# Kernel optimization log

Measured on AMD Instinct MI355X. Metric: run time of the kernel, lower is better.

The kernel has to match this reference:

```python
import jax, jax.numpy as jnp
import numpy as np

N_EMBD, D_INNER, DT_RANK, D_CONV, D_STATE, SEQ_LEN = 2048, 4096, 128, 4, 16, 2048


def setup_inputs() -> dict:
    key = jax.random.key(0)
    ks = jax.random.split(key, 8)
    sc = lambda fan_in: 1.0 / np.sqrt(fan_in)
    x = jax.random.normal(ks[0], (SEQ_LEN, N_EMBD), dtype=jnp.float32)
    in_proj_w = jax.random.normal(ks[1], (2 * D_INNER, N_EMBD), jnp.float32) * sc(N_EMBD)
    in_proj_b = jnp.zeros((2 * D_INNER,), jnp.float32)
    conv_w = jax.random.normal(ks[2], (D_INNER, 1, D_CONV), jnp.float32) * sc(D_CONV)
    conv_b = jnp.zeros((D_INNER,), jnp.float32)
    ssm_in_w = jax.random.normal(ks[3], (DT_RANK + 2 * D_STATE, D_INNER), jnp.float32) * sc(D_INNER)
    delta_w = jax.random.normal(ks[4], (D_INNER, DT_RANK), jnp.float32) * sc(DT_RANK)
    # A_log init exactly as module: repeat(arange(1,d_state+1), d_inner).reshape(d_inner,d_state)
    A_log = jnp.log(jnp.repeat(jnp.arange(1, D_STATE + 1), D_INNER).reshape(D_INNER, D_STATE).astype(jnp.float32))
    D = jnp.ones((D_INNER,), jnp.float32)
    out_w = jax.random.normal(ks[5], (N_EMBD, D_INNER), jnp.float32) * sc(D_INNER)
    out_b = jnp.zeros((N_EMBD,), jnp.float32)
    return {"x": x, "in_proj_w": in_proj_w, "in_proj_b": in_proj_b, "conv_w": conv_w,
            "conv_b": conv_b, "ssm_in_w": ssm_in_w, "delta_w": delta_w, "A_log": A_log,
            "D": D, "out_w": out_w, "out_b": out_b}


def selective_scan(u, delta, A, B, C, D):
    # u, delta: (L, di); A: (di, ds); B, C: (L, ds); D: (di,)
    dA = jnp.exp(delta[:, :, None] * A[None, :, :])                # (L, di, ds)
    dBu = delta[:, :, None] * B[:, None, :] * u[:, :, None]        # (L, di, ds)

    def step(h, inp):
        dA_t, dBu_t, C_t = inp
        h = dA_t * h + dBu_t                                       # (di, ds)
        y = jnp.einsum('ds,s->d', h, C_t)
        return h, y

    h0 = jnp.zeros((u.shape[1], A.shape[1]), u.dtype)
    _, ys = jax.lax.scan(step, h0, (dA, dBu, C))
    return ys + u * D                                              # (L, di)


def mamba_block(x, in_proj_w, in_proj_b, conv_w, conv_b, ssm_in_w, delta_w, A_log, D, out_w, out_b):
    L = x.shape[0]
    xr = x @ in_proj_w.T + in_proj_b                               # (L, 2*di)
    xi, res = jnp.split(xr, 2, axis=-1)
    # depthwise causal conv1d: left-pad d_conv-1 (== first L outputs of symmetric pad)
    xc = jax.lax.conv_general_dilated(
        xi.T[None],                                                # (1, di, L)
        conv_w,                                                    # (di, 1, k)
        window_strides=(1,), padding=[(D_CONV - 1, 0)],
        feature_group_count=D_INNER)[0] + conv_b[:, None]
    xc = jax.nn.silu(xc.T)                                         # (L, di)
    # SSM
    A = -jnp.exp(A_log)
    dbc = xc @ ssm_in_w.T                                          # (L, dt_rank + 2*ds)
    delta, B, C = jnp.split(dbc, [DT_RANK, DT_RANK + D_STATE], axis=-1)
    delta = jax.nn.softplus(delta @ delta_w.T)                     # (L, di)
    y = selective_scan(xc, delta, A, B, C, D)
    y = y * jax.nn.silu(res)
    return y @ out_w.T + out_b                                     # (L, n_embd)


def reference(x, in_proj_w, in_proj_b, conv_w, conv_b, ssm_in_w, delta_w, A_log, D, out_w, out_b):
    return mamba_block(x, in_proj_w, in_proj_b, conv_w, conv_b, ssm_in_w, delta_w, A_log, D, out_w, out_b)
```

## Files before the change

### kernel.cpp

```cpp
#include <hip/hip_runtime.h>
#include <cstdint>
#include <cstddef>


typedef __bf16 bf16x8 __attribute__((ext_vector_type(8)));
typedef float f32x4 __attribute__((ext_vector_type(4)));

#define GLDS16(g, l)                                        \
  __builtin_amdgcn_global_load_lds(                         \
      (__attribute__((address_space(1))) void*)(g),         \
      (__attribute__((address_space(3))) void*)(l), 16, 0, 0)

#define FENCE() asm volatile("" ::: "memory")
#define BARRIER()                      \
  do {                                 \
    FENCE();                           \
    __builtin_amdgcn_s_barrier();      \
    FENCE();                           \
  } while (0)

static __device__ __forceinline__ unsigned short f2b(float f) {
  unsigned int x = __builtin_bit_cast(unsigned int, f);
  x += 0x7fffu + ((x >> 16) & 1u);
  return (unsigned short)(x >> 16);
}

static __device__ __forceinline__ float b2f(unsigned short u) {
  return __builtin_bit_cast(float, (unsigned int)u << 16);
}

static __device__ __forceinline__ float sigmoidf_fast(float x) {
  return 1.0f / (1.0f + __expf(-x));
}

struct CastArgs {
  const float* src[5];
  unsigned short* dst[5];
  int n4[5];
};

__global__ __launch_bounds__(256) void cast_multi(CastArgs a) {
  const int stride = gridDim.x * 256;
  const int t = blockIdx.x * 256 + threadIdx.x;
#pragma unroll
  for (int k = 0; k < 5; ++k) {
    const float4* src = reinterpret_cast<const float4*>(a.src[k]);
    ushort4* dst = reinterpret_cast<ushort4*>(a.dst[k]);
    const int n4 = a.n4[k];
    for (int i = t; i < n4; i += stride) {
      float4 v = src[i];
      ushort4 o;
      o.x = f2b(v.x); o.y = f2b(v.y); o.z = f2b(v.z); o.w = f2b(v.w);
      dst[i] = o;
    }
  }
}

template <int MODE>
__global__ __launch_bounds__(512) void gemm256_bt(
    const unsigned short* __restrict__ A, const unsigned short* __restrict__ B,
    float* __restrict__ Cp, unsigned short* __restrict__ xib,
    unsigned short* __restrict__ rsb, const float* __restrict__ bias,
    int M, int N, int K, int Kslice) {
  __shared__ __align__(16) unsigned short lds[65536];
  const int tid = threadIdx.x;
  const int l = tid & 63;
  const int w = tid >> 6;
  const int wr = w >> 2;
  const int wc = w & 3;

  const int nwg = gridDim.x * gridDim.y;
  const int q = nwg >> 3;
  int flat = blockIdx.x + gridDim.x * blockIdx.y;
  flat = (flat & 7) * q + (flat >> 3);
  const int bx = flat % gridDim.x;
  const int by = flat / gridDim.x;

  const long brow = (long)bx * 256;
  const long bcol = (long)by * 256;
  const int ks = blockIdx.z;
  const int NT = Kslice >> 6;

  f32x4 acc[8][4] = {};

  const unsigned short* Ab = A + (size_t)brow * K + (size_t)ks * Kslice;
  const unsigned short* Bb = B + (size_t)bcol * K + (size_t)ks * Kslice;
  size_t soff[4];
  int doff[4];
#pragma unroll
  for (int i = 0; i < 4; ++i) {
    int idx = i * 512 + tid;
    int r = idx >> 3, s = idx & 7;
    soff[i] = (size_t)r * K + (size_t)((s ^ (r & 7)) << 3);
    doff[i] = idx * 8;
  }

  auto stage = [&](int kt, int buf) {
    const int k0 = kt << 6;
#pragma unroll
    for (int i = 0; i < 4; ++i)
      GLDS16(Ab + soff[i] + k0, &lds[buf * 32768 + doff[i]]);
#pragma unroll
    for (int i = 0; i < 4; ++i)
      GLDS16(Bb + soff[i] + k0, &lds[buf * 32768 + 16384 + doff[i]]);
  };

  const int hi = l >> 4, lo7 = l & 7;
  const int sw0 = ((0 + hi) ^ lo7) << 3;
  const int sw1 = ((4 + hi) ^ lo7) << 3;
  const int rowA = wr * 128 + (l & 15);
  const int colB = wc * 64 + (l & 15);

  stage(0, 0);
  stage(1, 1);

  int buf = 0;
  for (int kt = 0; kt < NT; ++kt) {
    const bool last = (kt == NT - 1);
    if (last) {
      asm volatile("s_waitcnt vmcnt(0)" ::: "memory");
    } else {
      asm volatile("s_waitcnt vmcnt(8)" ::: "memory");
    }
    BARRIER();
    const int bb = buf * 32768;
    bf16x8 a0[8], b0[4];
#pragma unroll
    for (int m = 0; m < 8; ++m)
      a0[m] = *reinterpret_cast<const bf16x8*>(&lds[bb + (rowA + m * 16) * 64 + sw0]);
#pragma unroll
    for (int n = 0; n < 4; ++n)
      b0[n] = *reinterpret_cast<const bf16x8*>(&lds[bb + 16384 + (colB + n * 16) * 64 + sw0]);
    __builtin_amdgcn_s_setprio(1);
#pragma unroll
    for (int m = 0; m < 8; ++m)
#pragma unroll
      for (int n = 0; n < 4; ++n)
        acc[m][n] = __builtin_amdgcn_mfma_f32_16x16x32_bf16(a0[m], b0[n], acc[m][n], 0, 0, 0);
    __builtin_amdgcn_s_setprio(0);
    bf16x8 a1[8], b1[4];
#pragma unroll
    for (int m = 0; m < 8; ++m)
      a1[m] = *reinterpret_cast<const bf16x8*>(&lds[bb + (rowA + m * 16) * 64 + sw1]);
#pragma unroll
    for (int n = 0; n < 4; ++n)
      b1[n] = *reinterpret_cast<const bf16x8*>(&lds[bb + 16384 + (colB + n * 16) * 64 + sw1]);
    asm volatile("s_waitcnt lgkmcnt(0)" ::: "memory");
    __builtin_amdgcn_sched_barrier(0);
    BARRIER();
    if (kt + 2 < NT) stage(kt + 2, buf);
    __builtin_amdgcn_s_setprio(1);
#pragma unroll
    for (int m = 0; m < 8; ++m)
#pragma unroll
      for (int n = 0; n < 4; ++n)
        acc[m][n] = __builtin_amdgcn_mfma_f32_16x16x32_bf16(a1[m], b1[n], acc[m][n], 0, 0, 0);
    __builtin_amdgcn_s_setprio(0);
    buf ^= 1;
  }

  const long r0 = brow + wr * 128 + (l >> 4) * 4;
  const long c0 = bcol + wc * 64 + (l & 15);
  if (MODE == 1) {
    float* Cb = Cp + (size_t)ks * M * N;
#pragma unroll
    for (int m = 0; m < 8; ++m)
#pragma unroll
      for (int n = 0; n < 4; ++n) {
        long col = c0 + n * 16;
#pragma unroll
        for (int r = 0; r < 4; ++r)
          Cb[(r0 + m * 16 + r) * (long)N + col] = acc[m][n][r];
      }
  } else {
#pragma unroll
    for (int m = 0; m < 8; ++m)
#pragma unroll
      for (int n = 0; n < 4; ++n) {
        long col = c0 + n * 16;
        float bv = bias[col];
        const bool isres = col >= 4096;
        long cc = isres ? col - 4096 : col;
#pragma unroll
        for (int r = 0; r < 4; ++r) {
          float v = acc[m][n][r] + bv;
          if (isres) {
            float s = v * sigmoidf_fast(v);
            rsb[(r0 + m * 16 + r) * 4096 + cc] = f2b(s);
          } else {
            xib[(r0 + m * 16 + r) * 4096 + cc] = f2b(v);
          }
        }
      }
  }
}

__global__ __launch_bounds__(512) void gemm128_bt(
    const unsigned short* __restrict__ A, const unsigned short* __restrict__ B,
    float* __restrict__ C, const float* __restrict__ bias,
    int M, int N, int K) {
  __shared__ __align__(16) unsigned short lds[32768];
  const int tid = threadIdx.x;
  const int l = tid & 63;
  const int w = tid >> 6;
  const int wr = w >> 2;
  const int wc = w & 3;

  const int nwg = gridDim.x * gridDim.y;
  const int q = nwg >> 3;
  int flat = blockIdx.x + gridDim.x * blockIdx.y;
  flat = (flat & 7) * q + (flat >> 3);
  const int bx = flat % gridDim.x;
  const int by = flat / gridDim.x;

  const long brow = (long)bx * 128;
  const long bcol = (long)by * 128;
  const int NT = K >> 6;

  f32x4 acc[4][2] = {};

  const unsigned short* Ab = A + (size_t)brow * K;
  const unsigned short* Bb = B + (size_t)bcol * K;
  size_t soff[2];
  int doff[2];
#pragma unroll
  for (int i = 0; i < 2; ++i) {
    int idx = i * 512 + tid;
    int r = idx >> 3, s = idx & 7;
    soff[i] = (size_t)r * K + (size_t)((s ^ (r & 7)) << 3);
    doff[i] = idx * 8;
  }

  auto stage = [&](int kt, int buf) {
    const int k0 = kt << 6;
#pragma unroll
    for (int i = 0; i < 2; ++i)
      GLDS16(Ab + soff[i] + k0, &lds[buf * 16384 + doff[i]]);
#pragma unroll
    for (int i = 0; i < 2; ++i)
      GLDS16(Bb + soff[i] + k0, &lds[buf * 16384 + 8192 + doff[i]]);
  };

  const int hi = l >> 4, lo7 = l & 7;
  const int sw0 = ((0 + hi) ^ lo7) << 3;
  const int sw1 = ((4 + hi) ^ lo7) << 3;
  const int rowA = wr * 64 + (l & 15);
  const int colB = wc * 32 + (l & 15);

  stage(0, 0);
  stage(1, 1);

  int buf = 0;
  for (int kt = 0; kt < NT; ++kt) {
    const bool last = (kt == NT - 1);
    if (last) {
      asm volatile("s_waitcnt vmcnt(0)" ::: "memory");
    } else {
      asm volatile("s_waitcnt vmcnt(4)" ::: "memory");
    }
    BARRIER();
    const int bb = buf * 16384;
    bf16x8 a0[4], b0[2];
#pragma unroll
    for (int m = 0; m < 4; ++m)
      a0[m] = *reinterpret_cast<const bf16x8*>(&lds[bb + (rowA + m * 16) * 64 + sw0]);
#pragma unroll
    for (int n = 0; n < 2; ++n)
      b0[n] = *reinterpret_cast<const bf16x8*>(&lds[bb + 8192 + (colB + n * 16) * 64 + sw0]);
    __builtin_amdgcn_s_setprio(1);
#pragma unroll
    for (int m = 0; m < 4; ++m)
#pragma unroll
      for (int n = 0; n < 2; ++n)
        acc[m][n] = __builtin_amdgcn_mfma_f32_16x16x32_bf16(a0[m], b0[n], acc[m][n], 0, 0, 0);
    __builtin_amdgcn_s_setprio(0);
    bf16x8 a1[4], b1[2];
#pragma unroll
    for (int m = 0; m < 4; ++m)
      a1[m] = *reinterpret_cast<const bf16x8*>(&lds[bb + (rowA + m * 16) * 64 + sw1]);
#pragma unroll
    for (int n = 0; n < 2; ++n)
      b1[n] = *reinterpret_cast<const bf16x8*>(&lds[bb + 8192 + (colB + n * 16) * 64 + sw1]);
    asm volatile("s_waitcnt lgkmcnt(0)" ::: "memory");
    __builtin_amdgcn_sched_barrier(0);
    BARRIER();
    if (kt + 2 < NT) stage(kt + 2, buf);
    __builtin_amdgcn_s_setprio(1);
#pragma unroll
    for (int m = 0; m < 4; ++m)
#pragma unroll
      for (int n = 0; n < 2; ++n)
        acc[m][n] = __builtin_amdgcn_mfma_f32_16x16x32_bf16(a1[m], b1[n], acc[m][n], 0, 0, 0);
    __builtin_amdgcn_s_setprio(0);
    buf ^= 1;
  }

  const long r0 = brow + wr * 64 + (l >> 4) * 4;
  const long c0 = bcol + wc * 32 + (l & 15);
#pragma unroll
  for (int m = 0; m < 4; ++m) {
#pragma unroll
    for (int n = 0; n < 2; ++n) {
      long col = c0 + n * 16;
      float bv = bias[col];
#pragma unroll
      for (int r = 0; r < 4; ++r)
        C[(r0 + m * 16 + r) * (long)N + col] = acc[m][n][r] + bv;
    }
  }
}

__global__ __launch_bounds__(256) void gemm_bt_sp(
    const unsigned short* __restrict__ A, const unsigned short* __restrict__ B,
    float* __restrict__ C, int M, int N, int K) {
  __shared__ __align__(16) unsigned short lA[128 * 32];
  __shared__ __align__(16) unsigned short lB[128 * 32];
  const int tid = threadIdx.x;
  const int l = tid & 63;
  const int w = tid >> 6;
  const int wr = w >> 1, wc = w & 1;
  const long brow = (long)blockIdx.x * 128;
  const long bcol = (long)blockIdx.y * 128;

  f32x4 acc[4][4] = {};

  const int srow = tid >> 2;
  const int scol = (tid & 3) * 8;

  const unsigned short* Ab = A + (size_t)brow * K;
  const unsigned short* Bb = B + (size_t)bcol * K;

  for (int k0 = 0; k0 < K; k0 += 32) {
#pragma unroll
    for (int j = 0; j < 2; ++j) {
      GLDS16(Ab + (size_t)(j * 64 + srow) * K + k0 + scol, &lA[j * 2048 + tid * 8]);
      GLDS16(Bb + (size_t)(j * 64 + srow) * K + k0 + scol, &lB[j * 2048 + tid * 8]);
    }
    __syncthreads();
    bf16x8 af[4], bfr[4];
#pragma unroll
    for (int mt = 0; mt < 4; ++mt)
      af[mt] = *reinterpret_cast<const bf16x8*>(
          &lA[(wr * 64 + mt * 16 + (l & 15)) * 32 + (l >> 4) * 8]);
#pragma unroll
    for (int nt = 0; nt < 4; ++nt)
      bfr[nt] = *reinterpret_cast<const bf16x8*>(
          &lB[(wc * 64 + nt * 16 + (l & 15)) * 32 + (l >> 4) * 8]);
#pragma unroll
    for (int mt = 0; mt < 4; ++mt)
#pragma unroll
      for (int nt = 0; nt < 4; ++nt)
        acc[mt][nt] = __builtin_amdgcn_mfma_f32_16x16x32_bf16(
            af[mt], bfr[nt], acc[mt][nt], 0, 0, 0);
    __syncthreads();
  }

  const long r0 = brow + wr * 64 + ((l >> 4) * 4);
  const long c0 = bcol + wc * 64 + (l & 15);
#pragma unroll
  for (int mt = 0; mt < 4; ++mt) {
#pragma unroll
    for (int nt = 0; nt < 4; ++nt) {
      long col = c0 + nt * 16;
#pragma unroll
      for (int r = 0; r < 4; ++r) {
        long row = r0 + mt * 16 + r;
        float v = acc[mt][nt][r];
        v = (v > 20.0f) ? v : log1pf(__expf(v));
        C[row * (long)N + col] = v;
      }
    }
  }
}

__global__ __launch_bounds__(256) void conv_silu_k(
    const unsigned short* __restrict__ xib, const float* __restrict__ cw,
    const float* __restrict__ cb, unsigned short* __restrict__ xcb) {
  const int d = blockIdx.x * 256 + threadIdx.x;
  const int t0 = blockIdx.y * 128;
  const float4 wv = *reinterpret_cast<const float4*>(cw + (size_t)d * 4);
  const float bv = cb[d];
  float xm3 = (t0 >= 3) ? b2f(xib[(size_t)(t0 - 3) * 4096 + d]) : 0.0f;
  float xm2 = (t0 >= 2) ? b2f(xib[(size_t)(t0 - 2) * 4096 + d]) : 0.0f;
  float xm1 = (t0 >= 1) ? b2f(xib[(size_t)(t0 - 1) * 4096 + d]) : 0.0f;
  for (int tt = 0; tt < 128; ++tt) {
    const size_t t = (size_t)t0 + tt;
    float xt = b2f(xib[t * 4096 + d]);
    float a = bv + wv.x * xm3 + wv.y * xm2 + wv.z * xm1 + wv.w * xt;
    float s = a * sigmoidf_fast(a);
    xcb[t * 4096 + d] = f2b(s);
    xm3 = xm2; xm2 = xm1; xm1 = xt;
  }
}

__global__ __launch_bounds__(256) void gemm_dbc(
    const unsigned short* __restrict__ A, const unsigned short* __restrict__ B,
    float* __restrict__ part) {
  __shared__ __align__(16) unsigned short lA[64 * 32];
  __shared__ __align__(16) unsigned short lB[160 * 32];
  const int tid = threadIdx.x;
  const int l = tid & 63, w = tid >> 6;
  const int brow = blockIdx.x * 64;
  const int ks = blockIdx.y;
  const int K = 4096;
  f32x4 acc[10] = {};
  const int srow = tid >> 2, scol = (tid & 3) * 8;
  for (int k0 = ks * 512; k0 < ks * 512 + 512; k0 += 32) {
    GLDS16(A + (size_t)(brow + srow) * K + k0 + scol, &lA[tid * 8]);
#pragma unroll
    for (int j = 0; j < 3; ++j) {
      int li = j * 256 + tid;
      if (li < 640) {
        GLDS16(B + (size_t)(li >> 2) * K + k0 + (li & 3) * 8, &lB[li * 8]);
      }
    }
    __syncthreads();
    bf16x8 af = *reinterpret_cast<const bf16x8*>(
        &lA[(w * 16 + (l & 15)) * 32 + (l >> 4) * 8]);
#pragma unroll
    for (int nt = 0; nt < 10; ++nt) {
      bf16x8 bfr = *reinterpret_cast<const bf16x8*>(
          &lB[(nt * 16 + (l & 15)) * 32 + (l >> 4) * 8]);
      acc[nt] = __builtin_amdgcn_mfma_f32_16x16x32_bf16(af, bfr, acc[nt], 0, 0, 0);
    }
    __syncthreads();
  }
  const int r0 = brow + w * 16 + (l >> 4) * 4;
  const int c = l & 15;
#pragma unroll
  for (int nt = 0; nt < 10; ++nt)
#pragma unroll
    for (int r = 0; r < 4; ++r)
      part[((size_t)ks * 2048 + r0 + r) * 160 + nt * 16 + c] = acc[nt][r];
}

__global__ __launch_bounds__(256) void reduce_dbc(
    const float* __restrict__ part, unsigned short* __restrict__ drb,
    float* __restrict__ bc) {
  int idx = blockIdx.x * 256 + threadIdx.x;
  float s = 0.0f;
#pragma unroll
  for (int k = 0; k < 8; ++k) s += part[(size_t)k * 2048 * 160 + idx];
  int row = idx / 160, col = idx - row * 160;
  if (col < 128) drb[row * 128 + col] = f2b(s);
  else bc[row * 32 + (col - 128)] = s;
}

__global__ __launch_bounds__(256) void scan_passA(
    const float* __restrict__ delta, const unsigned short* __restrict__ xcb,
    const float* __restrict__ bc, const float* __restrict__ alog,
    float* __restrict__ P, float* __restrict__ S) {
  __shared__ float lbc[1024];
  const int d = blockIdx.x * 256 + threadIdx.x;
  const int c = blockIdx.y;
  const int t0 = c * 32;
#pragma unroll
  for (int j = 0; j < 4; ++j) {
    int idx = j * 256 + threadIdx.x;
    lbc[idx] = bc[(size_t)t0 * 32 + idx];
  }
  __syncthreads();
  float a[16], h[16], p[16];
#pragma unroll
  for (int s = 0; s < 16; ++s) {
    a[s] = -__expf(alog[(size_t)d * 16 + s]);
    h[s] = 0.0f;
    p[s] = 1.0f;
  }
  for (int tt = 0; tt < 32; ++tt) {
    float dt = delta[(size_t)(t0 + tt) * 4096 + d];
    float u = b2f(xcb[(size_t)(t0 + tt) * 4096 + d]);
    float du = dt * u;
#pragma unroll
    for (int s = 0; s < 16; ++s) {
      float e = __expf(dt * a[s]);
      h[s] = e * h[s] + du * lbc[tt * 32 + s];
      p[s] *= e;
    }
  }
  size_t o = ((size_t)c * 4096 + d) * 16;
#pragma unroll
  for (int s = 0; s < 16; s += 4) {
    *reinterpret_cast<float4*>(&P[o + s]) = make_float4(p[s], p[s + 1], p[s + 2], p[s + 3]);
    *reinterpret_cast<float4*>(&S[o + s]) = make_float4(h[s], h[s + 1], h[s + 2], h[s + 3]);
  }
}

__global__ __launch_bounds__(256) void scan_passB(
    float* __restrict__ P, const float* __restrict__ S) {
  const int idx = blockIdx.x * 256 + threadIdx.x;
  float h = 0.0f;
  for (int c = 0; c < 64; ++c) {
    size_t o = (size_t)c * 65536 + idx;
    float p = P[o], sv = S[o];
    P[o] = h;
    h = p * h + sv;
  }
}

__global__ __launch_bounds__(256) void scan_passC(
    const float* __restrict__ delta, const unsigned short* __restrict__ xcb,
    const float* __restrict__ bc, const float* __restrict__ alog,
    const float* __restrict__ hst, const float* __restrict__ Dp,
    const unsigned short* __restrict__ rsb, unsigned short* __restrict__ yb) {
  __shared__ float lbc[1024];
  const int d = blockIdx.x * 256 + threadIdx.x;
  const int c = blockIdx.y;
  const int t0 = c * 32;
#pragma unroll
  for (int j = 0; j < 4; ++j) {
    int idx = j * 256 + threadIdx.x;
    lbc[idx] = bc[(size_t)t0 * 32 + idx];
  }
  __syncthreads();
  float a[16], h[16];
  size_t o = ((size_t)c * 4096 + d) * 16;
#pragma unroll
  for (int s = 0; s < 16; ++s) {
    a[s] = -__expf(alog[(size_t)d * 16 + s]);
    h[s] = hst[o + s];
  }
  const float Dv = Dp[d];
  for (int tt = 0; tt < 32; ++tt) {
    float dt = delta[(size_t)(t0 + tt) * 4096 + d];
    float u = b2f(xcb[(size_t)(t0 + tt) * 4096 + d]);
    float du = dt * u;
    float y = 0.0f;
#pragma unroll
    for (int s = 0; s < 16; ++s) {
      float e = __expf(dt * a[s]);
      h[s] = e * h[s] + du * lbc[tt * 32 + s];
      y += h[s] * lbc[tt * 32 + 16 + s];
    }
    float rs = b2f(rsb[(size_t)(t0 + tt) * 4096 + d]);
    float v = (y + u * Dv) * rs;
    yb[(size_t)(t0 + tt) * 4096 + d] = f2b(v);
  }
}

extern "C" void kernel_launch(void* const* d_in, const int* in_sizes, int n_in,
                              void* d_out, int out_size, void* d_ws, size_t ws_size,
                              hipStream_t stream) {
  const float* x    = (const float*)d_in[0];
  const float* w1   = (const float*)d_in[1];
  const float* b1   = (const float*)d_in[2];
  const float* cw   = (const float*)d_in[3];
  const float* cb   = (const float*)d_in[4];
  const float* w2   = (const float*)d_in[5];
  const float* w3   = (const float*)d_in[6];
  const float* alog = (const float*)d_in[7];
  const float* Dp   = (const float*)d_in[8];
  const float* w4   = (const float*)d_in[9];
  const float* b4   = (const float*)d_in[10];
  float* out = (float*)d_out;

  char* ws = (char*)d_ws;
  size_t off = 0;
  auto alloc = [&](size_t b) {
    size_t o = off;
    off += (b + 255) & ~(size_t)255;
    return o;
  };
  unsigned short* w1b = (unsigned short*)(ws + alloc(2ull * 8192 * 2048));
  unsigned short* xb  = (unsigned short*)(ws + alloc(2ull * 2048 * 2048));
  unsigned short* w2b = (unsigned short*)(ws + alloc(2ull * 160 * 4096));
  unsigned short* w3b = (unsigned short*)(ws + alloc(2ull * 4096 * 128));
  unsigned short* w4b = (unsigned short*)(ws + alloc(2ull * 2048 * 4096));
  unsigned short* xib = (unsigned short*)(ws + alloc(2ull * 2048 * 4096));
  unsigned short* rsb = (unsigned short*)(ws + alloc(2ull * 2048 * 4096));
  unsigned short* xcb = (unsigned short*)(ws + alloc(2ull * 2048 * 4096));
  unsigned short* drb = (unsigned short*)(ws + alloc(2ull * 2048 * 128));
  float* bcb  = (float*)(ws + alloc(4ull * 2048 * 32));
  float* delta = (float*)(ws + alloc(4ull * 2048 * 4096));
  float* P = (float*)(ws + alloc(4ull * 64 * 4096 * 16));
  float* S = (float*)(ws + alloc(4ull * 64 * 4096 * 16));
  float* part  = delta;
  unsigned short* yb = xib;

  if (ws_size < off) return;

  CastArgs ca;
  ca.src[0] = w1; ca.dst[0] = w1b; ca.n4[0] = 8192 * 2048 / 4;
  ca.src[1] = x;  ca.dst[1] = xb;  ca.n4[1] = 2048 * 2048 / 4;
  ca.src[2] = w2; ca.dst[2] = w2b; ca.n4[2] = 160 * 4096 / 4;
  ca.src[3] = w3; ca.dst[3] = w3b; ca.n4[3] = 4096 * 128 / 4;
  ca.src[4] = w4; ca.dst[4] = w4b; ca.n4[4] = 2048 * 4096 / 4;
  cast_multi<<<2048, 256, 0, stream>>>(ca);

  gemm256_bt<2><<<dim3(8, 32, 1), 512, 0, stream>>>(
      xb, w1b, nullptr, xib, rsb, b1, 2048, 8192, 2048, 2048);
  conv_silu_k<<<dim3(16, 16), 256, 0, stream>>>(xib, cw, cb, xcb);
  gemm_dbc<<<dim3(32, 8), 256, 0, stream>>>(xcb, w2b, part);
  reduce_dbc<<<1280, 256, 0, stream>>>(part, drb, bcb);
  gemm_bt_sp<<<dim3(16, 32), 256, 0, stream>>>(drb, w3b, delta, 2048, 4096, 128);
  scan_passA<<<dim3(16, 64), 256, 0, stream>>>(delta, xcb, bcb, alog, P, S);
  scan_passB<<<256, 256, 0, stream>>>(P, S);
  scan_passC<<<dim3(16, 64), 256, 0, stream>>>(delta, xcb, bcb, alog, P, Dp, rsb, yb);
  gemm128_bt<<<dim3(16, 16), 512, 0, stream>>>(yb, w4b, out, b4, 2048, 2048, 4096);
}
```

Baseline: 304.3 us.

## Store in_proj output as one interleaved buffer, move res SiLU into scan, use longer scan chunks

The first GEMM epilogue now writes biased bf16 results for both halves into a single 2048x8192 buffer, with no per-column branching. The SiLU on the residual half is moved into scan pass C, which reads the raw residual values. The chunked scan uses 32 chunks of 64 timesteps instead of 64 of 32, which halves the P/S state traffic and the pass-B serial loop. The cost is half as many scan blocks in passes A and C and a wider row stride for the conv and scan reads, which may lower parallelism and coalescing efficiency.

```diff
diff --git a/kernel.cpp b/kernel.cpp
--- a/kernel.cpp
+++ b/kernel.cpp
@@ -56,12 +56,10 @@
   }
 }
 
-template <int MODE>
-__global__ __launch_bounds__(512) void gemm256_bt(
+__global__ __launch_bounds__(512) void gemmG1(
     const unsigned short* __restrict__ A, const unsigned short* __restrict__ B,
-    float* __restrict__ Cp, unsigned short* __restrict__ xib,
-    unsigned short* __restrict__ rsb, const float* __restrict__ bias,
-    int M, int N, int K, int Kslice) {
+    unsigned short* __restrict__ xrb, const float* __restrict__ bias,
+    int M, int N, int K) {
   __shared__ __align__(16) unsigned short lds[65536];
   const int tid = threadIdx.x;
   const int l = tid & 63;
@@ -78,13 +76,12 @@
 
   const long brow = (long)bx * 256;
   const long bcol = (long)by * 256;
-  const int ks = blockIdx.z;
-  const int NT = Kslice >> 6;
+  const int NT = K >> 6;
 
   f32x4 acc[8][4] = {};
 
-  const unsigned short* Ab = A + (size_t)brow * K + (size_t)ks * Kslice;
-  const unsigned short* Bb = B + (size_t)bcol * K + (size_t)ks * Kslice;
+  const unsigned short* Ab = A + (size_t)brow * K;
+  const unsigned short* Bb = B + (size_t)bcol * K;
   size_t soff[4];
   int doff[4];
 #pragma unroll
@@ -161,37 +158,16 @@
 
   const long r0 = brow + wr * 128 + (l >> 4) * 4;
   const long c0 = bcol + wc * 64 + (l & 15);
-  if (MODE == 1) {
-    float* Cb = Cp + (size_t)ks * M * N;
-#pragma unroll
-    for (int m = 0; m < 8; ++m)
-#pragma unroll
-      for (int n = 0; n < 4; ++n) {
-        long col = c0 + n * 16;
-#pragma unroll
-        for (int r = 0; r < 4; ++r)
-          Cb[(r0 + m * 16 + r) * (long)N + col] = acc[m][n][r];
-      }
-  } else {
-#pragma unroll
-    for (int m = 0; m < 8; ++m)
-#pragma unroll
-      for (int n = 0; n < 4; ++n) {
-        long col = c0 + n * 16;
-        float bv = bias[col];
-        const bool isres = col >= 4096;
-        long cc = isres ? col - 4096 : col;
-#pragma unroll
-        for (int r = 0; r < 4; ++r) {
-          float v = acc[m][n][r] + bv;
-          if (isres) {
-            float s = v * sigmoidf_fast(v);
-            rsb[(r0 + m * 16 + r) * 4096 + cc] = f2b(s);
-          } else {
-            xib[(r0 + m * 16 + r) * 4096 + cc] = f2b(v);
-          }
-        }
-      }
+#pragma unroll
+  for (int m = 0; m < 8; ++m) {
+#pragma unroll
+    for (int n = 0; n < 4; ++n) {
+      const long col = c0 + n * 16;
+      const float bv = bias[col];
+#pragma unroll
+      for (int r = 0; r < 4; ++r)
+        xrb[(r0 + m * 16 + r) * (long)N + col] = f2b(acc[m][n][r] + bv);
+    }
   }
 }
 
@@ -374,18 +350,18 @@
 }
 
 __global__ __launch_bounds__(256) void conv_silu_k(
-    const unsigned short* __restrict__ xib, const float* __restrict__ cw,
+    const unsigned short* __restrict__ xrb, const float* __restrict__ cw,
     const float* __restrict__ cb, unsigned short* __restrict__ xcb) {
   const int d = blockIdx.x * 256 + threadIdx.x;
   const int t0 = blockIdx.y * 128;
   const float4 wv = *reinterpret_cast<const float4*>(cw + (size_t)d * 4);
   const float bv = cb[d];
-  float xm3 = (t0 >= 3) ? b2f(xib[(size_t)(t0 - 3) * 4096 + d]) : 0.0f;
-  float xm2 = (t0 >= 2) ? b2f(xib[(size_t)(t0 - 2) * 4096 + d]) : 0.0f;
-  float xm1 = (t0 >= 1) ? b2f(xib[(size_t)(t0 - 1) * 4096 + d]) : 0.0f;
+  float xm3 = (t0 >= 3) ? b2f(xrb[(size_t)(t0 - 3) * 8192 + d]) : 0.0f;
+  float xm2 = (t0 >= 2) ? b2f(xrb[(size_t)(t0 - 2) * 8192 + d]) : 0.0f;
+  float xm1 = (t0 >= 1) ? b2f(xrb[(size_t)(t0 - 1) * 8192 + d]) : 0.0f;
   for (int tt = 0; tt < 128; ++tt) {
     const size_t t = (size_t)t0 + tt;
-    float xt = b2f(xib[t * 4096 + d]);
+    float xt = b2f(xrb[t * 8192 + d]);
     float a = bv + wv.x * xm3 + wv.y * xm2 + wv.z * xm1 + wv.w * xt;
     float s = a * sigmoidf_fast(a);
     xcb[t * 4096 + d] = f2b(s);
@@ -450,12 +426,12 @@
     const float* __restrict__ delta, const unsigned short* __restrict__ xcb,
     const float* __restrict__ bc, const float* __restrict__ alog,
     float* __restrict__ P, float* __restrict__ S) {
-  __shared__ float lbc[1024];
+  __shared__ float lbc[2048];
   const int d = blockIdx.x * 256 + threadIdx.x;
   const int c = blockIdx.y;
-  const int t0 = c * 32;
-#pragma unroll
-  for (int j = 0; j < 4; ++j) {
+  const int t0 = c * 64;
+#pragma unroll
+  for (int j = 0; j < 8; ++j) {
     int idx = j * 256 + threadIdx.x;
     lbc[idx] = bc[(size_t)t0 * 32 + idx];
   }
@@ -467,7 +443,7 @@
     h[s] = 0.0f;
     p[s] = 1.0f;
   }
-  for (int tt = 0; tt < 32; ++tt) {
+  for (int tt = 0; tt < 64; ++tt) {
     float dt = delta[(size_t)(t0 + tt) * 4096 + d];
     float u = b2f(xcb[(size_t)(t0 + tt) * 4096 + d]);
     float du = dt * u;
@@ -490,7 +466,7 @@
     float* __restrict__ P, const float* __restrict__ S) {
   const int idx = blockIdx.x * 256 + threadIdx.x;
   float h = 0.0f;
-  for (int c = 0; c < 64; ++c) {
+  for (int c = 0; c < 32; ++c) {
     size_t o = (size_t)c * 65536 + idx;
     float p = P[o], sv = S[o];
     P[o] = h;
@@ -502,13 +478,13 @@
     const float* __restrict__ delta, const unsigned short* __restrict__ xcb,
     const float* __restrict__ bc, const float* __restrict__ alog,
     const float* __restrict__ hst, const float* __restrict__ Dp,
-    const unsigned short* __restrict__ rsb, unsigned short* __restrict__ yb) {
-  __shared__ float lbc[1024];
+    const unsigned short* __restrict__ xrb, unsigned short* __restrict__ yb) {
+  __shared__ float lbc[2048];
   const int d = blockIdx.x * 256 + threadIdx.x;
   const int c = blockIdx.y;
-  const int t0 = c * 32;
-#pragma unroll
-  for (int j = 0; j < 4; ++j) {
+  const int t0 = c * 64;
+#pragma unroll
+  for (int j = 0; j < 8; ++j) {
     int idx = j * 256 + threadIdx.x;
     lbc[idx] = bc[(size_t)t0 * 32 + idx];
   }
@@ -521,7 +497,7 @@
     h[s] = hst[o + s];
   }
   const float Dv = Dp[d];
-  for (int tt = 0; tt < 32; ++tt) {
+  for (int tt = 0; tt < 64; ++tt) {
     float dt = delta[(size_t)(t0 + tt) * 4096 + d];
     float u = b2f(xcb[(size_t)(t0 + tt) * 4096 + d]);
     float du = dt * u;
@@ -532,7 +508,8 @@
       h[s] = e * h[s] + du * lbc[tt * 32 + s];
       y += h[s] * lbc[tt * 32 + 16 + s];
     }
-    float rs = b2f(rsb[(size_t)(t0 + tt) * 4096 + d]);
+    float res = b2f(xrb[(size_t)(t0 + tt) * 8192 + 4096 + d]);
+    float rs = res * sigmoidf_fast(res);
     float v = (y + u * Dv) * rs;
     yb[(size_t)(t0 + tt) * 4096 + d] = f2b(v);
   }
@@ -566,16 +543,15 @@
   unsigned short* w2b = (unsigned short*)(ws + alloc(2ull * 160 * 4096));
   unsigned short* w3b = (unsigned short*)(ws + alloc(2ull * 4096 * 128));
   unsigned short* w4b = (unsigned short*)(ws + alloc(2ull * 2048 * 4096));
-  unsigned short* xib = (unsigned short*)(ws + alloc(2ull * 2048 * 4096));
-  unsigned short* rsb = (unsigned short*)(ws + alloc(2ull * 2048 * 4096));
+  unsigned short* xrb = (unsigned short*)(ws + alloc(2ull * 2048 * 8192));
   unsigned short* xcb = (unsigned short*)(ws + alloc(2ull * 2048 * 4096));
   unsigned short* drb = (unsigned short*)(ws + alloc(2ull * 2048 * 128));
   float* bcb  = (float*)(ws + alloc(4ull * 2048 * 32));
   float* delta = (float*)(ws + alloc(4ull * 2048 * 4096));
-  float* P = (float*)(ws + alloc(4ull * 64 * 4096 * 16));
-  float* S = (float*)(ws + alloc(4ull * 64 * 4096 * 16));
+  float* P = (float*)(ws + alloc(4ull * 32 * 4096 * 16));
+  float* S = (float*)(ws + alloc(4ull * 32 * 4096 * 16));
+  unsigned short* yb = (unsigned short*)(ws + alloc(2ull * 2048 * 4096));
   float* part  = delta;
-  unsigned short* yb = xib;
 
   if (ws_size < off) return;
 
@@ -587,14 +563,13 @@
   ca.src[4] = w4; ca.dst[4] = w4b; ca.n4[4] = 2048 * 4096 / 4;
   cast_multi<<<2048, 256, 0, stream>>>(ca);
 
-  gemm256_bt<2><<<dim3(8, 32, 1), 512, 0, stream>>>(
-      xb, w1b, nullptr, xib, rsb, b1, 2048, 8192, 2048, 2048);
-  conv_silu_k<<<dim3(16, 16), 256, 0, stream>>>(xib, cw, cb, xcb);
+  gemmG1<<<dim3(8, 32), 512, 0, stream>>>(xb, w1b, xrb, b1, 2048, 8192, 2048);
+  conv_silu_k<<<dim3(16, 16), 256, 0, stream>>>(xrb, cw, cb, xcb);
   gemm_dbc<<<dim3(32, 8), 256, 0, stream>>>(xcb, w2b, part);
   reduce_dbc<<<1280, 256, 0, stream>>>(part, drb, bcb);
   gemm_bt_sp<<<dim3(16, 32), 256, 0, stream>>>(drb, w3b, delta, 2048, 4096, 128);
-  scan_passA<<<dim3(16, 64), 256, 0, stream>>>(delta, xcb, bcb, alog, P, S);
+  scan_passA<<<dim3(16, 32), 256, 0, stream>>>(delta, xcb, bcb, alog, P, S);
   scan_passB<<<256, 256, 0, stream>>>(P, S);
-  scan_passC<<<dim3(16, 64), 256, 0, stream>>>(delta, xcb, bcb, alog, P, Dp, rsb, yb);
+  scan_passC<<<dim3(16, 32), 256, 0, stream>>>(delta, xcb, bcb, alog, P, Dp, xrb, yb);
   gemm128_bt<<<dim3(16, 16), 512, 0, stream>>>(yb, w4b, out, b4, 2048, 2048, 4096);
 }
```

Result: slower. 311.5 us (+2.4%).
